# Kernel optimization log

Hardware: AMD Instinct MI355X
Metric: run time of the kernel (lower is better)

Reference implementation:

```python
import jax, jax.numpy as jnp
import numpy as np

B, LQ, LK = 8, 64, 256
E, H, D, NH = 128, 4, 32, 128  # embed_time, num_heads, input_dim, nhidden
EK = E // H


def setup_inputs() -> dict:
    key = jax.random.key(0)
    ks = jax.random.split(key, 10)
    s = 1.0 / np.sqrt(E)
    so = 1.0 / np.sqrt(D * H)
    return {
        "query": jax.random.normal(ks[0], (B, LQ, E), jnp.float32),
        "key": jax.random.normal(ks[1], (B, LK, E), jnp.float32),
        "value": jax.random.normal(ks[2], (B, LK, D), jnp.float32),
        "mask": jax.random.randint(ks[3], (B, LK, D), 0, 2, jnp.int32),
        "Wq": jax.random.uniform(ks[4], (E, E), jnp.float32, -s, s),
        "bq": jax.random.uniform(ks[5], (E,), jnp.float32, -s, s),
        "Wk": jax.random.uniform(ks[6], (E, E), jnp.float32, -s, s),
        "bk": jax.random.uniform(ks[7], (E,), jnp.float32, -s, s),
        "Wo": jax.random.uniform(ks[8], (D * H, NH), jnp.float32, -so, so),
        "bo": jax.random.uniform(ks[9], (NH,), jnp.float32, -so, so),
    }


def reference(query, key, value, mask, Wq, bq, Wk, bk, Wo, bo):
    # project and split heads: [B, L, E] -> [B, H, L, EK]
    q = (query @ Wq + bq).reshape(B, LQ, H, EK).transpose(0, 2, 1, 3)
    k = (key @ Wk + bk).reshape(B, LK, H, EK).transpose(0, 2, 1, 3)
    # scores: [B, H, LQ, LK]
    scores = jnp.einsum("bhqe,bhke->bhqk", q, k) / jnp.sqrt(jnp.asarray(EK, q.dtype))
    # per-feature masked logits: [B, H, LQ, LK, D] (broadcast, matches repeat_interleave)
    m = mask[:, None, None, :, :]  # [B,1,1,LK,D]
    logits = jnp.where(m == 0, jnp.asarray(-1e9, q.dtype), scores[..., None])
    p = jax.nn.softmax(logits, axis=-2)  # softmax over LK, per feature channel
    # weighted sum over LK: [B, H, LQ, D]
    x = jnp.sum(p * value[:, None, None, :, :], axis=-2)
    # merge heads: [B, LQ, H*D]
    x = x.transpose(0, 2, 1, 3).reshape(B, LQ, H * D)
    return x @ Wo + bo
```

## Files before the change

kernel.cpp:

```cpp
#include <hip/hip_runtime.h>

#define B_ 8
#define LQ_ 64
#define LK_ 256
#define E_ 128
#define H_ 4
#define D_ 32
#define NH_ 128
#define EK_ 32

__global__ __launch_bounds__(512, 2) void fused_attn_kernel(
    const float* __restrict__ query, const float* __restrict__ key,
    const float* __restrict__ value, const int* __restrict__ mask,
    const float* __restrict__ Wq, const float* __restrict__ bq,
    const float* __restrict__ Wk,
    const float* __restrict__ Wo, const float* __restrict__ bo,
    float* __restrict__ out)
{
    const int blk = blockIdx.x;
    const int b  = blk >> 5;
    const int q0 = (blk & 31) * 2;
    const int t  = threadIdx.x;

    extern __shared__ float dyn[];
    float* qrow  = dyn;
    float* qpart = dyn + 256;
    float* qp    = dyn + 1280;
    float* g     = dyn + 1536;
    float* kt    = dyn + 2560;
    float* spart = dyn + 2560;
    float* e_lds = dyn + 10752;
    float* nump  = dyn + 12800;
    float* denp  = dyn + 16896;
    float* x     = dyn + 20992;
    float* opart = dyn + 21248;

    {
        const float4* kb4 =
            reinterpret_cast<const float4*>(key + (size_t)b * LK_ * E_);
        #pragma unroll
        for (int i = 0; i < 16; ++i) {
            const int slot = i * 512 + t;
            const int k  = slot >> 5;
            const int p  = slot & 31;
            const float4* src = kb4 + (k * 32 + (p ^ (k & 7)));
            __builtin_amdgcn_global_load_lds(
                (const __attribute__((address_space(1))) void*)src,
                (__attribute__((address_space(3))) void*)(&kt[slot * 4]),
                16, 0, 0);
        }
    }

    const int d  = t & 31;
    const int kg = t >> 5;
    float vv[16], mfv[16];
    {
        const float* vb = value + ((size_t)(b * LK_) + kg * 16) * D_ + d;
        const int*   mb = mask  + ((size_t)(b * LK_) + kg * 16) * D_ + d;
        #pragma unroll
        for (int j = 0; j < 16; ++j) {
            vv[j]  = vb[j * D_];
            mfv[j] = (float)mb[j * D_];
        }
    }

    const int e4 = t >> 2, p4 = t & 3;
    float4 wkr[8];
    {
        const float4* wk4 =
            reinterpret_cast<const float4*>(Wk + (size_t)e4 * E_ + p4 * EK_);
        #pragma unroll
        for (int j = 0; j < 8; ++j) wkr[j] = wk4[j];
    }

    if (t < 64) {
        reinterpret_cast<float4*>(qrow)[t] =
            reinterpret_cast<const float4*>(query + ((size_t)(b * LQ_) + q0) * E_)[t];
    }
    __syncthreads();

    {
        const int col  = t & 127;
        const int slab = t >> 7;
        const float4* qr0 = reinterpret_cast<const float4*>(qrow + slab * 32);
        const float4* qr1 = reinterpret_cast<const float4*>(qrow + 128 + slab * 32);
        const float* wq = Wq + (size_t)(slab * 32) * E_ + col;
        float acc0 = 0.0f, acc1 = 0.0f;
        #pragma unroll
        for (int j = 0; j < 8; ++j) {
            float4 q0v = qr0[j];
            float4 q1v = qr1[j];
            float w0 = wq[(size_t)(j * 4 + 0) * E_];
            float w1 = wq[(size_t)(j * 4 + 1) * E_];
            float w2 = wq[(size_t)(j * 4 + 2) * E_];
            float w3 = wq[(size_t)(j * 4 + 3) * E_];
            acc0 = fmaf(q0v.x, w0, acc0); acc1 = fmaf(q1v.x, w0, acc1);
            acc0 = fmaf(q0v.y, w1, acc0); acc1 = fmaf(q1v.y, w1, acc1);
            acc0 = fmaf(q0v.z, w2, acc0); acc1 = fmaf(q1v.z, w2, acc1);
            acc0 = fmaf(q0v.w, w3, acc0); acc1 = fmaf(q1v.w, w3, acc1);
        }
        qpart[(slab * 2 + 0) * 128 + col] = acc0;
        qpart[(slab * 2 + 1) * 128 + col] = acc1;
    }
    __syncthreads();

    if (t < 256) {
        const int col = t & 127, r = t >> 7;
        float s = bq[col];
        #pragma unroll
        for (int slab = 0; slab < 4; ++slab)
            s += qpart[(slab * 2 + r) * 128 + col];
        qp[r * 128 + col] = s;
    }
    __syncthreads();

    {
        const float inv_sqrt_ek = 0.17677669529663687f;
        #pragma unroll
        for (int r = 0; r < 2; ++r) {
            const float4* qp4 = reinterpret_cast<const float4*>(qp + r * 128 + p4 * EK_);
            float acc = 0.0f;
            #pragma unroll
            for (int j = 0; j < 8; ++j) {
                float4 pv = qp4[j];
                acc = fmaf(wkr[j].x, pv.x, acc);
                acc = fmaf(wkr[j].y, pv.y, acc);
                acc = fmaf(wkr[j].z, pv.z, acc);
                acc = fmaf(wkr[j].w, pv.w, acc);
            }
            g[(r * 4 + p4) * 128 + e4] = acc * inv_sqrt_ek;
        }
    }
    __syncthreads();

    const int k5  = t & 127;
    const int eq5 = t >> 7;
    float acc0[8] = {0.f, 0.f, 0.f, 0.f, 0.f, 0.f, 0.f, 0.f};
    float acc1[8] = {0.f, 0.f, 0.f, 0.f, 0.f, 0.f, 0.f, 0.f};
    {
        const int xr = k5 & 7;
        const float4* kt4 = reinterpret_cast<const float4*>(kt);
        const float4* g4  = reinterpret_cast<const float4*>(g);
        #pragma unroll
        for (int j = 0; j < 8; ++j) {
            const int jj = eq5 * 8 + j;
            const float4 kv0 = kt4[k5 * 32 + (jj ^ xr)];
            const float4 kv1 = kt4[(k5 + 128) * 32 + (jj ^ xr)];
            #pragma unroll
            for (int rh = 0; rh < 8; ++rh) {
                const float4 gg = g4[rh * 32 + jj];
                acc0[rh] = fmaf(kv0.x, gg.x, acc0[rh]);
                acc0[rh] = fmaf(kv0.y, gg.y, acc0[rh]);
                acc0[rh] = fmaf(kv0.z, gg.z, acc0[rh]);
                acc0[rh] = fmaf(kv0.w, gg.w, acc0[rh]);
                acc1[rh] = fmaf(kv1.x, gg.x, acc1[rh]);
                acc1[rh] = fmaf(kv1.y, gg.y, acc1[rh]);
                acc1[rh] = fmaf(kv1.z, gg.z, acc1[rh]);
                acc1[rh] = fmaf(kv1.w, gg.w, acc1[rh]);
            }
        }
    }
    __syncthreads();

    #pragma unroll
    for (int rh = 0; rh < 8; ++rh) {
        spart[(eq5 * 8 + rh) * 256 + k5]       = acc0[rh];
        spart[(eq5 * 8 + rh) * 256 + k5 + 128] = acc1[rh];
    }
    __syncthreads();

    {
        const int w = t >> 6;
        const int l = t & 63;
        const float4* sp4 = reinterpret_cast<const float4*>(spart);
        float4 s0 = sp4[w * 64 + l];
        #pragma unroll
        for (int eq = 1; eq < 4; ++eq) {
            float4 s1 = sp4[(eq * 8 + w) * 64 + l];
            s0.x += s1.x; s0.y += s1.y; s0.z += s1.z; s0.w += s1.w;
        }
        float m = fmaxf(fmaxf(s0.x, s0.y), fmaxf(s0.z, s0.w));
        #pragma unroll
        for (int off = 32; off; off >>= 1)
            m = fmaxf(m, __shfl_xor(m, off));
        float4 e;
        e.x = __expf(s0.x - m); e.y = __expf(s0.y - m);
        e.z = __expf(s0.z - m); e.w = __expf(s0.w - m);
        *reinterpret_cast<float4*>(&e_lds[w * LK_ + l * 4]) = e;
    }
    __syncthreads();

    {
        float num[8] = {0.f, 0.f, 0.f, 0.f, 0.f, 0.f, 0.f, 0.f};
        float den[8] = {0.f, 0.f, 0.f, 0.f, 0.f, 0.f, 0.f, 0.f};
        #pragma unroll
        for (int jq = 0; jq < 4; ++jq) {
            const float4 mv4 = make_float4(mfv[jq*4+0]*vv[jq*4+0], mfv[jq*4+1]*vv[jq*4+1],
                                           mfv[jq*4+2]*vv[jq*4+2], mfv[jq*4+3]*vv[jq*4+3]);
            const float4 mf4 = make_float4(mfv[jq*4+0], mfv[jq*4+1],
                                           mfv[jq*4+2], mfv[jq*4+3]);
            #pragma unroll
            for (int rh = 0; rh < 8; ++rh) {
                float4 ev = *reinterpret_cast<const float4*>(
                    &e_lds[rh * LK_ + kg * 16 + jq * 4]);
                num[rh] = fmaf(ev.x, mv4.x, num[rh]);
                num[rh] = fmaf(ev.y, mv4.y, num[rh]);
                num[rh] = fmaf(ev.z, mv4.z, num[rh]);
                num[rh] = fmaf(ev.w, mv4.w, num[rh]);
                den[rh] = fmaf(ev.x, mf4.x, den[rh]);
                den[rh] = fmaf(ev.y, mf4.y, den[rh]);
                den[rh] = fmaf(ev.z, mf4.z, den[rh]);
                den[rh] = fmaf(ev.w, mf4.w, den[rh]);
            }
        }
        #pragma unroll
        for (int rh = 0; rh < 8; ++rh) {
            nump[(kg * 8 + rh) * 32 + d] = num[rh];
            denp[(kg * 8 + rh) * 32 + d] = den[rh];
        }
    }
    __syncthreads();

    if (t < 256) {
        const int rh = t >> 5, dd = t & 31;
        float n = 0.f, dn = 0.f;
        #pragma unroll
        for (int k2 = 0; k2 < 16; ++k2) {
            n  += nump[(k2 * 8 + rh) * 32 + dd];
            dn += denp[(k2 * 8 + rh) * 32 + dd];
        }
        x[(rh >> 2) * 128 + (rh & 3) * 32 + dd] = n / dn;
    }
    __syncthreads();

    {
        const int col = t & 127;
        const int eq  = t >> 7;
        const int c0  = eq * 32;
        const float* wo = Wo + (size_t)c0 * NH_ + col;
        const float4* x40 = reinterpret_cast<const float4*>(x + c0);
        const float4* x41 = reinterpret_cast<const float4*>(x + 128 + c0);
        float acc0o = 0.f, acc1o = 0.f;
        #pragma unroll
        for (int j = 0; j < 8; ++j) {
            float4 xv0 = x40[j];
            float4 xv1 = x41[j];
            float w0 = wo[(size_t)(j * 4 + 0) * NH_];
            float w1 = wo[(size_t)(j * 4 + 1) * NH_];
            float w2 = wo[(size_t)(j * 4 + 2) * NH_];
            float w3 = wo[(size_t)(j * 4 + 3) * NH_];
            acc0o = fmaf(xv0.x, w0, acc0o); acc1o = fmaf(xv1.x, w0, acc1o);
            acc0o = fmaf(xv0.y, w1, acc0o); acc1o = fmaf(xv1.y, w1, acc1o);
            acc0o = fmaf(xv0.z, w2, acc0o); acc1o = fmaf(xv1.z, w2, acc1o);
            acc0o = fmaf(xv0.w, w3, acc0o); acc1o = fmaf(xv1.w, w3, acc1o);
        }
        opart[(eq * 2 + 0) * 128 + col] = acc0o;
        opart[(eq * 2 + 1) * 128 + col] = acc1o;
    }
    __syncthreads();

    if (t < 256) {
        const int col = t & 127, r = t >> 7;
        float s = bo[col];
        #pragma unroll
        for (int eq = 0; eq < 4; ++eq)
            s += opart[(eq * 2 + r) * 128 + col];
        out[((size_t)(b * LQ_) + q0 + r) * NH_ + col] = s;
    }
}

extern "C" void kernel_launch(void* const* d_in, const int* in_sizes, int n_in,
                              void* d_out, int out_size, void* d_ws, size_t ws_size,
                              hipStream_t stream) {
    const float* query = (const float*)d_in[0];
    const float* key   = (const float*)d_in[1];
    const float* value = (const float*)d_in[2];
    const int*   mask  = (const int*)d_in[3];
    const float* Wq    = (const float*)d_in[4];
    const float* bq    = (const float*)d_in[5];
    const float* Wk    = (const float*)d_in[6];
    const float* Wo    = (const float*)d_in[8];
    const float* bo    = (const float*)d_in[9];
    float* out = (float*)d_out;

    const size_t lds_bytes = 35328 * sizeof(float);
    static bool attr_set = false;
    if (!attr_set) {
        hipFuncSetAttribute(reinterpret_cast<const void*>(fused_attn_kernel),
                            hipFuncAttributeMaxDynamicSharedMemorySize,
                            (int)lds_bytes);
        attr_set = true;
    }

    fused_attn_kernel<<<B_ * (LQ_ / 2), 512, lds_bytes, stream>>>(
        query, key, value, mask, Wq, bq, Wk, Wo, bo, out);
}
```

Before: 16.32 us.

## Split projections into separate kernel and compute scores from projected keys

Adds a proj_kernel that computes the Q and K projections into workspace: K is scaled by 1/sqrt(EK) and Q gets its bias. The attention kernel then loads the projected K and computes scores as direct per-head dot products. This replaces the per-block folding of Wk into the query (the g vectors), which needed 8 head-row accumulators and a 4-way partial-sum reduction. It removes the K projection work that was redundantly repeated across the 32 query blocks per batch. The cost is a second kernel launch and a global round trip through workspace, and the fused kernel remains as a fallback when no workspace is given. It also drops the bk bias, relying on the fact that adding bk shifts each score row by a constant that softmax cancels.

```diff
diff --git a/kernel.cpp b/kernel.cpp
--- a/kernel.cpp
+++ b/kernel.cpp
@@ -9,11 +9,61 @@
 #define NH_ 128
 #define EK_ 32
 
-__global__ __launch_bounds__(512, 2) void fused_attn_kernel(
-    const float* __restrict__ query, const float* __restrict__ key,
+#define SCALE_EK 0.17677669529663687f
+
+
+__global__ __launch_bounds__(256, 4) void proj_kernel(
+    const float* __restrict__ key, const float* __restrict__ query,
+    const float* __restrict__ Wk, const float* __restrict__ Wq,
+    const float* __restrict__ bq,
+    float* __restrict__ kp, float* __restrict__ qp)
+{
+    const int blkrow = blockIdx.x * 4;
+    const int t = threadIdx.x;
+    const bool is_q = blkrow >= (B_ * LK_);
+    const float* in = is_q ? (query + (size_t)(blkrow - B_ * LK_) * E_)
+                           : (key + (size_t)blkrow * E_);
+    const float* W = is_q ? Wq : Wk;
+
+    __shared__ float in_lds[4 * E_];
+    if (t < 128)
+        reinterpret_cast<float4*>(in_lds)[t] =
+            reinterpret_cast<const float4*>(in)[t];
+    __syncthreads();
+
+    const int col = t & 127;
+    const int rr  = t >> 7;
+    const float4* i40 = reinterpret_cast<const float4*>(in_lds + rr * E_);
+    const float4* i41 = reinterpret_cast<const float4*>(in_lds + (rr + 2) * E_);
+    float acc0 = 0.f, acc1 = 0.f;
+    #pragma unroll
+    for (int jf = 0; jf < 32; ++jf) {
+        const float4 a0 = i40[jf];
+        const float4 a1 = i41[jf];
+        const float* wr = W + (size_t)(jf * 4) * E_ + col;
+        const float w0 = wr[0];
+        const float w1 = wr[E_];
+        const float w2 = wr[2 * E_];
+        const float w3 = wr[3 * E_];
+        acc0 = fmaf(a0.x, w0, acc0); acc1 = fmaf(a1.x, w0, acc1);
+        acc0 = fmaf(a0.y, w1, acc0); acc1 = fmaf(a1.y, w1, acc1);
+        acc0 = fmaf(a0.z, w2, acc0); acc1 = fmaf(a1.z, w2, acc1);
+        acc0 = fmaf(a0.w, w3, acc0); acc1 = fmaf(a1.w, w3, acc1);
+    }
+    if (is_q) {
+        const int r0 = blkrow - B_ * LK_;
+        const float bb = bq[col];
+        qp[(size_t)(r0 + rr) * E_ + col]     = acc0 + bb;
+        qp[(size_t)(r0 + rr + 2) * E_ + col] = acc1 + bb;
+    } else {
+        kp[(size_t)(blkrow + rr) * E_ + col]     = acc0 * SCALE_EK;
+        kp[(size_t)(blkrow + rr + 2) * E_ + col] = acc1 * SCALE_EK;
+    }
+}
+
+__global__ __launch_bounds__(512, 2) void attn_kernel(
+    const float* __restrict__ kp, const float* __restrict__ qp_g,
     const float* __restrict__ value, const int* __restrict__ mask,
-    const float* __restrict__ Wq, const float* __restrict__ bq,
-    const float* __restrict__ Wk,
     const float* __restrict__ Wo, const float* __restrict__ bo,
     float* __restrict__ out)
 {
@@ -23,26 +73,23 @@
     const int t  = threadIdx.x;
 
     extern __shared__ float dyn[];
-    float* qrow  = dyn;
-    float* qpart = dyn + 256;
-    float* qp    = dyn + 1280;
-    float* g     = dyn + 1536;
-    float* kt    = dyn + 2560;
-    float* spart = dyn + 2560;
-    float* e_lds = dyn + 10752;
-    float* nump  = dyn + 12800;
-    float* denp  = dyn + 16896;
-    float* x     = dyn + 20992;
-    float* opart = dyn + 21248;
+    float* qp_lds = dyn;
+    float* s_lds  = dyn + 256;
+    float* kt     = dyn + 2560;
+    float* e_lds  = dyn + 2560;
+    float* nump   = dyn + 4608;
+    float* denp   = dyn + 8704;
+    float* x      = dyn + 12800;
+    float* opart  = dyn + 13056;
 
     {
         const float4* kb4 =
-            reinterpret_cast<const float4*>(key + (size_t)b * LK_ * E_);
+            reinterpret_cast<const float4*>(kp + (size_t)b * LK_ * E_);
         #pragma unroll
         for (int i = 0; i < 16; ++i) {
             const int slot = i * 512 + t;
-            const int k  = slot >> 5;
-            const int p  = slot & 31;
+            const int k = slot >> 5;
+            const int p = slot & 31;
             const float4* src = kb4 + (k * 32 + (p ^ (k & 7)));
             __builtin_amdgcn_global_load_lds(
                 (const __attribute__((address_space(1))) void*)src,
@@ -64,121 +111,47 @@
         }
     }
 
-    const int e4 = t >> 2, p4 = t & 3;
-    float4 wkr[8];
-    {
-        const float4* wk4 =
-            reinterpret_cast<const float4*>(Wk + (size_t)e4 * E_ + p4 * EK_);
-        #pragma unroll
-        for (int j = 0; j < 8; ++j) wkr[j] = wk4[j];
-    }
-
     if (t < 64) {
-        reinterpret_cast<float4*>(qrow)[t] =
-            reinterpret_cast<const float4*>(query + ((size_t)(b * LQ_) + q0) * E_)[t];
-    }
-    __syncthreads();
-
-    {
-        const int col  = t & 127;
-        const int slab = t >> 7;
-        const float4* qr0 = reinterpret_cast<const float4*>(qrow + slab * 32);
-        const float4* qr1 = reinterpret_cast<const float4*>(qrow + 128 + slab * 32);
-        const float* wq = Wq + (size_t)(slab * 32) * E_ + col;
-        float acc0 = 0.0f, acc1 = 0.0f;
-        #pragma unroll
-        for (int j = 0; j < 8; ++j) {
-            float4 q0v = qr0[j];
-            float4 q1v = qr1[j];
-            float w0 = wq[(size_t)(j * 4 + 0) * E_];
-            float w1 = wq[(size_t)(j * 4 + 1) * E_];
-            float w2 = wq[(size_t)(j * 4 + 2) * E_];
-            float w3 = wq[(size_t)(j * 4 + 3) * E_];
-            acc0 = fmaf(q0v.x, w0, acc0); acc1 = fmaf(q1v.x, w0, acc1);
-            acc0 = fmaf(q0v.y, w1, acc0); acc1 = fmaf(q1v.y, w1, acc1);
-            acc0 = fmaf(q0v.z, w2, acc0); acc1 = fmaf(q1v.z, w2, acc1);
-            acc0 = fmaf(q0v.w, w3, acc0); acc1 = fmaf(q1v.w, w3, acc1);
-        }
-        qpart[(slab * 2 + 0) * 128 + col] = acc0;
-        qpart[(slab * 2 + 1) * 128 + col] = acc1;
-    }
-    __syncthreads();
-
-    if (t < 256) {
-        const int col = t & 127, r = t >> 7;
-        float s = bq[col];
-        #pragma unroll
-        for (int slab = 0; slab < 4; ++slab)
-            s += qpart[(slab * 2 + r) * 128 + col];
-        qp[r * 128 + col] = s;
-    }
-    __syncthreads();
-
-    {
-        const float inv_sqrt_ek = 0.17677669529663687f;
-        #pragma unroll
-        for (int r = 0; r < 2; ++r) {
-            const float4* qp4 = reinterpret_cast<const float4*>(qp + r * 128 + p4 * EK_);
-            float acc = 0.0f;
-            #pragma unroll
-            for (int j = 0; j < 8; ++j) {
-                float4 pv = qp4[j];
-                acc = fmaf(wkr[j].x, pv.x, acc);
-                acc = fmaf(wkr[j].y, pv.y, acc);
-                acc = fmaf(wkr[j].z, pv.z, acc);
-                acc = fmaf(wkr[j].w, pv.w, acc);
-            }
-            g[(r * 4 + p4) * 128 + e4] = acc * inv_sqrt_ek;
-        }
-    }
-    __syncthreads();
-
-    const int k5  = t & 127;
-    const int eq5 = t >> 7;
-    float acc0[8] = {0.f, 0.f, 0.f, 0.f, 0.f, 0.f, 0.f, 0.f};
-    float acc1[8] = {0.f, 0.f, 0.f, 0.f, 0.f, 0.f, 0.f, 0.f};
-    {
+        reinterpret_cast<float4*>(qp_lds)[t] =
+            reinterpret_cast<const float4*>(qp_g + ((size_t)(b * LQ_) + q0) * E_)[t];
+    }
+    __syncthreads();
+
+    {
+        const int k5 = t & 127;
+        const int h5 = t >> 7;
         const int xr = k5 & 7;
         const float4* kt4 = reinterpret_cast<const float4*>(kt);
-        const float4* g4  = reinterpret_cast<const float4*>(g);
+        const float4* q40 = reinterpret_cast<const float4*>(qp_lds + h5 * EK_);
+        const float4* q41 = reinterpret_cast<const float4*>(qp_lds + 128 + h5 * EK_);
+        float a00 = 0.f, a01 = 0.f, a10 = 0.f, a11 = 0.f;
         #pragma unroll
         for (int j = 0; j < 8; ++j) {
-            const int jj = eq5 * 8 + j;
+            const int jj = h5 * 8 + j;
             const float4 kv0 = kt4[k5 * 32 + (jj ^ xr)];
             const float4 kv1 = kt4[(k5 + 128) * 32 + (jj ^ xr)];
-            #pragma unroll
-            for (int rh = 0; rh < 8; ++rh) {
-                const float4 gg = g4[rh * 32 + jj];
-                acc0[rh] = fmaf(kv0.x, gg.x, acc0[rh]);
-                acc0[rh] = fmaf(kv0.y, gg.y, acc0[rh]);
-                acc0[rh] = fmaf(kv0.z, gg.z, acc0[rh]);
-                acc0[rh] = fmaf(kv0.w, gg.w, acc0[rh]);
-                acc1[rh] = fmaf(kv1.x, gg.x, acc1[rh]);
-                acc1[rh] = fmaf(kv1.y, gg.y, acc1[rh]);
-                acc1[rh] = fmaf(kv1.z, gg.z, acc1[rh]);
-                acc1[rh] = fmaf(kv1.w, gg.w, acc1[rh]);
-            }
-        }
-    }
-    __syncthreads();
-
-    #pragma unroll
-    for (int rh = 0; rh < 8; ++rh) {
-        spart[(eq5 * 8 + rh) * 256 + k5]       = acc0[rh];
-        spart[(eq5 * 8 + rh) * 256 + k5 + 128] = acc1[rh];
+            const float4 qa = q40[j];
+            const float4 qb = q41[j];
+            a00 = fmaf(kv0.x, qa.x, a00); a01 = fmaf(kv1.x, qa.x, a01);
+            a00 = fmaf(kv0.y, qa.y, a00); a01 = fmaf(kv1.y, qa.y, a01);
+            a00 = fmaf(kv0.z, qa.z, a00); a01 = fmaf(kv1.z, qa.z, a01);
+            a00 = fmaf(kv0.w, qa.w, a00); a01 = fmaf(kv1.w, qa.w, a01);
+            a10 = fmaf(kv0.x, qb.x, a10); a11 = fmaf(kv1.x, qb.x, a11);
+            a10 = fmaf(kv0.y, qb.y, a10); a11 = fmaf(kv1.y, qb.y, a11);
+            a10 = fmaf(kv0.z, qb.z, a10); a11 = fmaf(kv1.z, qb.z, a11);
+            a10 = fmaf(kv0.w, qb.w, a10); a11 = fmaf(kv1.w, qb.w, a11);
+        }
+        s_lds[h5 * 256 + k5]             = a00;
+        s_lds[h5 * 256 + k5 + 128]       = a01;
+        s_lds[(4 + h5) * 256 + k5]       = a10;
+        s_lds[(4 + h5) * 256 + k5 + 128] = a11;
     }
     __syncthreads();
 
     {
         const int w = t >> 6;
         const int l = t & 63;
-        const float4* sp4 = reinterpret_cast<const float4*>(spart);
-        float4 s0 = sp4[w * 64 + l];
-        #pragma unroll
-        for (int eq = 1; eq < 4; ++eq) {
-            float4 s1 = sp4[(eq * 8 + w) * 64 + l];
-            s0.x += s1.x; s0.y += s1.y; s0.z += s1.z; s0.w += s1.w;
-        }
+        float4 s0 = *reinterpret_cast<const float4*>(&s_lds[w * 256 + l * 4]);
         float m = fmaxf(fmaxf(s0.x, s0.y), fmaxf(s0.z, s0.w));
         #pragma unroll
         for (int off = 32; off; off >>= 1)
@@ -240,6 +213,266 @@
         const float* wo = Wo + (size_t)c0 * NH_ + col;
         const float4* x40 = reinterpret_cast<const float4*>(x + c0);
         const float4* x41 = reinterpret_cast<const float4*>(x + 128 + c0);
+        float acc0 = 0.f, acc1 = 0.f;
+        #pragma unroll
+        for (int j = 0; j < 8; ++j) {
+            float4 xv0 = x40[j];
+            float4 xv1 = x41[j];
+            float w0 = wo[(size_t)(j * 4 + 0) * NH_];
+            float w1 = wo[(size_t)(j * 4 + 1) * NH_];
+            float w2 = wo[(size_t)(j * 4 + 2) * NH_];
+            float w3 = wo[(size_t)(j * 4 + 3) * NH_];
+            acc0 = fmaf(xv0.x, w0, acc0); acc1 = fmaf(xv1.x, w0, acc1);
+            acc0 = fmaf(xv0.y, w1, acc0); acc1 = fmaf(xv1.y, w1, acc1);
+            acc0 = fmaf(xv0.z, w2, acc0); acc1 = fmaf(xv1.z, w2, acc1);
+            acc0 = fmaf(xv0.w, w3, acc0); acc1 = fmaf(xv1.w, w3, acc1);
+        }
+        opart[(eq * 2 + 0) * 128 + col] = acc0;
+        opart[(eq * 2 + 1) * 128 + col] = acc1;
+    }
+    __syncthreads();
+
+    if (t < 256) {
+        const int col = t & 127, r = t >> 7;
+        float s = bo[col];
+        #pragma unroll
+        for (int eq = 0; eq < 4; ++eq)
+            s += opart[(eq * 2 + r) * 128 + col];
+        out[((size_t)(b * LQ_) + q0 + r) * NH_ + col] = s;
+    }
+}
+
+__global__ __launch_bounds__(512, 2) void fused_attn_kernel(
+    const float* __restrict__ query, const float* __restrict__ key,
+    const float* __restrict__ value, const int* __restrict__ mask,
+    const float* __restrict__ Wq, const float* __restrict__ bq,
+    const float* __restrict__ Wk,
+    const float* __restrict__ Wo, const float* __restrict__ bo,
+    float* __restrict__ out)
+{
+    const int blk = blockIdx.x;
+    const int b  = blk >> 5;
+    const int q0 = (blk & 31) * 2;
+    const int t  = threadIdx.x;
+
+    extern __shared__ float dyn[];
+    float* qrow  = dyn;
+    float* qpart = dyn + 256;
+    float* qp    = dyn + 1280;
+    float* g     = dyn + 1536;
+    float* kt    = dyn + 2560;
+    float* spart = dyn + 2560;
+    float* e_lds = dyn + 10752;
+    float* nump  = dyn + 12800;
+    float* denp  = dyn + 16896;
+    float* x     = dyn + 20992;
+    float* opart = dyn + 21248;
+
+    {
+        const float4* kb4 =
+            reinterpret_cast<const float4*>(key + (size_t)b * LK_ * E_);
+        #pragma unroll
+        for (int i = 0; i < 16; ++i) {
+            const int slot = i * 512 + t;
+            const int k  = slot >> 5;
+            const int p  = slot & 31;
+            const float4* src = kb4 + (k * 32 + (p ^ (k & 7)));
+            __builtin_amdgcn_global_load_lds(
+                (const __attribute__((address_space(1))) void*)src,
+                (__attribute__((address_space(3))) void*)(&kt[slot * 4]),
+                16, 0, 0);
+        }
+    }
+
+    const int d  = t & 31;
+    const int kg = t >> 5;
+    float vv[16], mfv[16];
+    {
+        const float* vb = value + ((size_t)(b * LK_) + kg * 16) * D_ + d;
+        const int*   mb = mask  + ((size_t)(b * LK_) + kg * 16) * D_ + d;
+        #pragma unroll
+        for (int j = 0; j < 16; ++j) {
+            vv[j]  = vb[j * D_];
+            mfv[j] = (float)mb[j * D_];
+        }
+    }
+
+    const int e4 = t >> 2, p4 = t & 3;
+    float4 wkr[8];
+    {
+        const float4* wk4 =
+            reinterpret_cast<const float4*>(Wk + (size_t)e4 * E_ + p4 * EK_);
+        #pragma unroll
+        for (int j = 0; j < 8; ++j) wkr[j] = wk4[j];
+    }
+
+    if (t < 64) {
+        reinterpret_cast<float4*>(qrow)[t] =
+            reinterpret_cast<const float4*>(query + ((size_t)(b * LQ_) + q0) * E_)[t];
+    }
+    __syncthreads();
+
+    {
+        const int col  = t & 127;
+        const int slab = t >> 7;
+        const float4* qr0 = reinterpret_cast<const float4*>(qrow + slab * 32);
+        const float4* qr1 = reinterpret_cast<const float4*>(qrow + 128 + slab * 32);
+        const float* wq = Wq + (size_t)(slab * 32) * E_ + col;
+        float acc0 = 0.0f, acc1 = 0.0f;
+        #pragma unroll
+        for (int j = 0; j < 8; ++j) {
+            float4 q0v = qr0[j];
+            float4 q1v = qr1[j];
+            float w0 = wq[(size_t)(j * 4 + 0) * E_];
+            float w1 = wq[(size_t)(j * 4 + 1) * E_];
+            float w2 = wq[(size_t)(j * 4 + 2) * E_];
+            float w3 = wq[(size_t)(j * 4 + 3) * E_];
+            acc0 = fmaf(q0v.x, w0, acc0); acc1 = fmaf(q1v.x, w0, acc1);
+            acc0 = fmaf(q0v.y, w1, acc0); acc1 = fmaf(q1v.y, w1, acc1);
+            acc0 = fmaf(q0v.z, w2, acc0); acc1 = fmaf(q1v.z, w2, acc1);
+            acc0 = fmaf(q0v.w, w3, acc0); acc1 = fmaf(q1v.w, w3, acc1);
+        }
+        qpart[(slab * 2 + 0) * 128 + col] = acc0;
+        qpart[(slab * 2 + 1) * 128 + col] = acc1;
+    }
+    __syncthreads();
+
+    if (t < 256) {
+        const int col = t & 127, r = t >> 7;
+        float s = bq[col];
+        #pragma unroll
+        for (int slab = 0; slab < 4; ++slab)
+            s += qpart[(slab * 2 + r) * 128 + col];
+        qp[r * 128 + col] = s;
+    }
+    __syncthreads();
+
+    {
+        const float inv_sqrt_ek = 0.17677669529663687f;
+        #pragma unroll
+        for (int r = 0; r < 2; ++r) {
+            const float4* qp4 = reinterpret_cast<const float4*>(qp + r * 128 + p4 * EK_);
+            float acc = 0.0f;
+            #pragma unroll
+            for (int j = 0; j < 8; ++j) {
+                float4 pv = qp4[j];
+                acc = fmaf(wkr[j].x, pv.x, acc);
+                acc = fmaf(wkr[j].y, pv.y, acc);
+                acc = fmaf(wkr[j].z, pv.z, acc);
+                acc = fmaf(wkr[j].w, pv.w, acc);
+            }
+            g[(r * 4 + p4) * 128 + e4] = acc * inv_sqrt_ek;
+        }
+    }
+    __syncthreads();
+
+    const int k5  = t & 127;
+    const int eq5 = t >> 7;
+    float acc0[8] = {0.f, 0.f, 0.f, 0.f, 0.f, 0.f, 0.f, 0.f};
+    float acc1[8] = {0.f, 0.f, 0.f, 0.f, 0.f, 0.f, 0.f, 0.f};
+    {
+        const int xr = k5 & 7;
+        const float4* kt4 = reinterpret_cast<const float4*>(kt);
+        const float4* g4  = reinterpret_cast<const float4*>(g);
+        #pragma unroll
+        for (int j = 0; j < 8; ++j) {
+            const int jj = eq5 * 8 + j;
+            const float4 kv0 = kt4[k5 * 32 + (jj ^ xr)];
+            const float4 kv1 = kt4[(k5 + 128) * 32 + (jj ^ xr)];
+            #pragma unroll
+            for (int rh = 0; rh < 8; ++rh) {
+                const float4 gg = g4[rh * 32 + jj];
+                acc0[rh] = fmaf(kv0.x, gg.x, acc0[rh]);
+                acc0[rh] = fmaf(kv0.y, gg.y, acc0[rh]);
+                acc0[rh] = fmaf(kv0.z, gg.z, acc0[rh]);
+                acc0[rh] = fmaf(kv0.w, gg.w, acc0[rh]);
+                acc1[rh] = fmaf(kv1.x, gg.x, acc1[rh]);
+                acc1[rh] = fmaf(kv1.y, gg.y, acc1[rh]);
+                acc1[rh] = fmaf(kv1.z, gg.z, acc1[rh]);
+                acc1[rh] = fmaf(kv1.w, gg.w, acc1[rh]);
+            }
+        }
+    }
+    __syncthreads();
+
+    #pragma unroll
+    for (int rh = 0; rh < 8; ++rh) {
+        spart[(eq5 * 8 + rh) * 256 + k5]       = acc0[rh];
+        spart[(eq5 * 8 + rh) * 256 + k5 + 128] = acc1[rh];
+    }
+    __syncthreads();
+
+    {
+        const int w = t >> 6;
+        const int l = t & 63;
+        const float4* sp4 = reinterpret_cast<const float4*>(spart);
+        float4 s0 = sp4[w * 64 + l];
+        #pragma unroll
+        for (int eq = 1; eq < 4; ++eq) {
+            float4 s1 = sp4[(eq * 8 + w) * 64 + l];
+            s0.x += s1.x; s0.y += s1.y; s0.z += s1.z; s0.w += s1.w;
+        }
+        float m = fmaxf(fmaxf(s0.x, s0.y), fmaxf(s0.z, s0.w));
+        #pragma unroll
+        for (int off = 32; off; off >>= 1)
+            m = fmaxf(m, __shfl_xor(m, off));
+        float4 e;
+        e.x = __expf(s0.x - m); e.y = __expf(s0.y - m);
+        e.z = __expf(s0.z - m); e.w = __expf(s0.w - m);
+        *reinterpret_cast<float4*>(&e_lds[w * LK_ + l * 4]) = e;
+    }
+    __syncthreads();
+
+    {
+        float num[8] = {0.f, 0.f, 0.f, 0.f, 0.f, 0.f, 0.f, 0.f};
+        float den[8] = {0.f, 0.f, 0.f, 0.f, 0.f, 0.f, 0.f, 0.f};
+        #pragma unroll
+        for (int jq = 0; jq < 4; ++jq) {
+            const float4 mv4 = make_float4(mfv[jq*4+0]*vv[jq*4+0], mfv[jq*4+1]*vv[jq*4+1],
+                                           mfv[jq*4+2]*vv[jq*4+2], mfv[jq*4+3]*vv[jq*4+3]);
+            const float4 mf4 = make_float4(mfv[jq*4+0], mfv[jq*4+1],
+                                           mfv[jq*4+2], mfv[jq*4+3]);
+            #pragma unroll
+            for (int rh = 0; rh < 8; ++rh) {
+                float4 ev = *reinterpret_cast<const float4*>(
+                    &e_lds[rh * LK_ + kg * 16 + jq * 4]);
+                num[rh] = fmaf(ev.x, mv4.x, num[rh]);
+                num[rh] = fmaf(ev.y, mv4.y, num[rh]);
+                num[rh] = fmaf(ev.z, mv4.z, num[rh]);
+                num[rh] = fmaf(ev.w, mv4.w, num[rh]);
+                den[rh] = fmaf(ev.x, mf4.x, den[rh]);
+                den[rh] = fmaf(ev.y, mf4.y, den[rh]);
+                den[rh] = fmaf(ev.z, mf4.z, den[rh]);
+                den[rh] = fmaf(ev.w, mf4.w, den[rh]);
+            }
+        }
+        #pragma unroll
+        for (int rh = 0; rh < 8; ++rh) {
+            nump[(kg * 8 + rh) * 32 + d] = num[rh];
+            denp[(kg * 8 + rh) * 32 + d] = den[rh];
+        }
+    }
+    __syncthreads();
+
+    if (t < 256) {
+        const int rh = t >> 5, dd = t & 31;
+        float n = 0.f, dn = 0.f;
+        #pragma unroll
+        for (int k2 = 0; k2 < 16; ++k2) {
+            n  += nump[(k2 * 8 + rh) * 32 + dd];
+            dn += denp[(k2 * 8 + rh) * 32 + dd];
+        }
+        x[(rh >> 2) * 128 + (rh & 3) * 32 + dd] = n / dn;
+    }
+    __syncthreads();
+
+    {
+        const int col = t & 127;
+        const int eq  = t >> 7;
+        const int c0  = eq * 32;
+        const float* wo = Wo + (size_t)c0 * NH_ + col;
+        const float4* x40 = reinterpret_cast<const float4*>(x + c0);
+        const float4* x41 = reinterpret_cast<const float4*>(x + 128 + c0);
         float acc0o = 0.f, acc1o = 0.f;
         #pragma unroll
         for (int j = 0; j < 8; ++j) {
@@ -284,14 +517,28 @@
     float* out = (float*)d_out;
 
     const size_t lds_bytes = 35328 * sizeof(float);
+    const size_t ws_needed = (size_t)(B_ * LK_ + B_ * LQ_) * E_ * sizeof(float);
+
     static bool attr_set = false;
     if (!attr_set) {
+        hipFuncSetAttribute(reinterpret_cast<const void*>(attn_kernel),
+                            hipFuncAttributeMaxDynamicSharedMemorySize,
+                            (int)lds_bytes);
         hipFuncSetAttribute(reinterpret_cast<const void*>(fused_attn_kernel),
                             hipFuncAttributeMaxDynamicSharedMemorySize,
                             (int)lds_bytes);
         attr_set = true;
     }
 
-    fused_attn_kernel<<<B_ * (LQ_ / 2), 512, lds_bytes, stream>>>(
-        query, key, value, mask, Wq, bq, Wk, Wo, bo, out);
+    if (d_ws != nullptr && ws_size >= ws_needed) {
+        float* kp = (float*)d_ws;
+        float* qp = kp + (size_t)B_ * LK_ * E_;
+        proj_kernel<<<(B_ * (LK_ + LQ_)) / 4, 256, 0, stream>>>(
+            key, query, Wk, Wq, bq, kp, qp);
+        attn_kernel<<<B_ * (LQ_ / 2), 512, lds_bytes, stream>>>(
+            kp, qp, value, mask, Wo, bo, out);
+    } else {
+        fused_attn_kernel<<<B_ * (LQ_ / 2), 512, lds_bytes, stream>>>(
+            query, key, value, mask, Wq, bq, Wk, Wo, bo, out);
+    }
 }
```

After: 18.01 us. 10.4% more time.

## Prefetch Wq/Wo weights into registers early, remap blocks, use raw barriers

Applied to the files above, without the earlier changes.

The Wq and Wo column slices are loaded into registers at kernel start, and the query row is loaded alongside the key-to-LDS copy, so the global latency of these loads overlaps instead of sitting on the critical path of each projection. The block index is permuted so that consecutive blocks spread across batches. Several __syncthreads are replaced with an inline s_waitcnt lgkmcnt(0)+s_barrier that does not wait on outstanding vector memory loads, which lets the in-flight global_load_lds key copy continue through the early barriers. The cost is 64 extra live registers per thread under launch_bounds(512,2), which risks spills, and the raw barrier relies on the LDS-loaded key data being waited on correctly later.

```diff
diff --git a/kernel.cpp b/kernel.cpp
--- a/kernel.cpp
+++ b/kernel.cpp
@@ -9,6 +9,9 @@
 #define NH_ 128
 #define EK_ 32
 
+
+#define RAW_BARRIER() asm volatile("s_waitcnt lgkmcnt(0)\n\ts_barrier" ::: "memory")
+
 __global__ __launch_bounds__(512, 2) void fused_attn_kernel(
     const float* __restrict__ query, const float* __restrict__ key,
     const float* __restrict__ value, const int* __restrict__ mask,
@@ -17,7 +20,8 @@
     const float* __restrict__ Wo, const float* __restrict__ bo,
     float* __restrict__ out)
 {
-    const int blk = blockIdx.x;
+    const int blk0 = blockIdx.x;
+    const int blk  = (blk0 & 7) * 32 + (blk0 >> 3);
     const int b  = blk >> 5;
     const int q0 = (blk & 31) * 2;
     const int t  = threadIdx.x;
@@ -35,14 +39,37 @@
     float* x     = dyn + 20992;
     float* opart = dyn + 21248;
 
+    float4 qv0;
+    if (t < 64)
+        qv0 = reinterpret_cast<const float4*>(
+            query + ((size_t)(b * LQ_) + q0) * E_)[t];
+
+    const int col2  = t & 127;
+    const int slab2 = t >> 7;
+    float wqr[32];
+    {
+        const float* wqp = Wq + (size_t)(slab2 * 32) * E_ + col2;
+        #pragma unroll
+        for (int j = 0; j < 32; ++j) wqr[j] = wqp[(size_t)j * E_];
+    }
+
+    const int e4 = t >> 2, p4 = t & 3;
+    float4 wkr[8];
+    {
+        const float4* wk4 =
+            reinterpret_cast<const float4*>(Wk + (size_t)e4 * E_ + p4 * EK_);
+        #pragma unroll
+        for (int j = 0; j < 8; ++j) wkr[j] = wk4[j];
+    }
+
     {
         const float4* kb4 =
             reinterpret_cast<const float4*>(key + (size_t)b * LK_ * E_);
         #pragma unroll
         for (int i = 0; i < 16; ++i) {
             const int slot = i * 512 + t;
-            const int k  = slot >> 5;
-            const int p  = slot & 31;
+            const int k = slot >> 5;
+            const int p = slot & 31;
             const float4* src = kb4 + (k * 32 + (p ^ (k & 7)));
             __builtin_amdgcn_global_load_lds(
                 (const __attribute__((address_space(1))) void*)src,
@@ -64,45 +91,39 @@
         }
     }
 
-    const int e4 = t >> 2, p4 = t & 3;
-    float4 wkr[8];
-    {
-        const float4* wk4 =
-            reinterpret_cast<const float4*>(Wk + (size_t)e4 * E_ + p4 * EK_);
-        #pragma unroll
-        for (int j = 0; j < 8; ++j) wkr[j] = wk4[j];
+    float wor[32];
+    {
+        const float* wop = Wo + (size_t)(slab2 * 32) * NH_ + col2;
+        #pragma unroll
+        for (int j = 0; j < 32; ++j) wor[j] = wop[(size_t)j * NH_];
     }
 
     if (t < 64) {
-        reinterpret_cast<float4*>(qrow)[t] =
-            reinterpret_cast<const float4*>(query + ((size_t)(b * LQ_) + q0) * E_)[t];
-    }
-    __syncthreads();
-
-    {
-        const int col  = t & 127;
-        const int slab = t >> 7;
-        const float4* qr0 = reinterpret_cast<const float4*>(qrow + slab * 32);
-        const float4* qr1 = reinterpret_cast<const float4*>(qrow + 128 + slab * 32);
-        const float* wq = Wq + (size_t)(slab * 32) * E_ + col;
+        reinterpret_cast<float4*>(qrow)[t] = qv0;
+    }
+    RAW_BARRIER();
+
+    {
+        const float4* qr0 = reinterpret_cast<const float4*>(qrow + slab2 * 32);
+        const float4* qr1 = reinterpret_cast<const float4*>(qrow + 128 + slab2 * 32);
         float acc0 = 0.0f, acc1 = 0.0f;
         #pragma unroll
         for (int j = 0; j < 8; ++j) {
             float4 q0v = qr0[j];
             float4 q1v = qr1[j];
-            float w0 = wq[(size_t)(j * 4 + 0) * E_];
-            float w1 = wq[(size_t)(j * 4 + 1) * E_];
-            float w2 = wq[(size_t)(j * 4 + 2) * E_];
-            float w3 = wq[(size_t)(j * 4 + 3) * E_];
+            const float w0 = wqr[j * 4 + 0];
+            const float w1 = wqr[j * 4 + 1];
+            const float w2 = wqr[j * 4 + 2];
+            const float w3 = wqr[j * 4 + 3];
             acc0 = fmaf(q0v.x, w0, acc0); acc1 = fmaf(q1v.x, w0, acc1);
             acc0 = fmaf(q0v.y, w1, acc0); acc1 = fmaf(q1v.y, w1, acc1);
             acc0 = fmaf(q0v.z, w2, acc0); acc1 = fmaf(q1v.z, w2, acc1);
             acc0 = fmaf(q0v.w, w3, acc0); acc1 = fmaf(q1v.w, w3, acc1);
         }
-        qpart[(slab * 2 + 0) * 128 + col] = acc0;
-        qpart[(slab * 2 + 1) * 128 + col] = acc1;
-    }
-    __syncthreads();
+        qpart[(slab2 * 2 + 0) * 128 + col2] = acc0;
+        qpart[(slab2 * 2 + 1) * 128 + col2] = acc1;
+    }
+    RAW_BARRIER();
 
     if (t < 256) {
         const int col = t & 127, r = t >> 7;
@@ -112,7 +133,7 @@
             s += qpart[(slab * 2 + r) * 128 + col];
         qp[r * 128 + col] = s;
     }
-    __syncthreads();
+    RAW_BARRIER();
 
     {
         const float inv_sqrt_ek = 0.17677669529663687f;
@@ -234,10 +255,7 @@
     __syncthreads();
 
     {
-        const int col = t & 127;
-        const int eq  = t >> 7;
-        const int c0  = eq * 32;
-        const float* wo = Wo + (size_t)c0 * NH_ + col;
+        const int c0 = slab2 * 32;
         const float4* x40 = reinterpret_cast<const float4*>(x + c0);
         const float4* x41 = reinterpret_cast<const float4*>(x + 128 + c0);
         float acc0o = 0.f, acc1o = 0.f;
@@ -245,17 +263,17 @@
         for (int j = 0; j < 8; ++j) {
             float4 xv0 = x40[j];
             float4 xv1 = x41[j];
-            float w0 = wo[(size_t)(j * 4 + 0) * NH_];
-            float w1 = wo[(size_t)(j * 4 + 1) * NH_];
-            float w2 = wo[(size_t)(j * 4 + 2) * NH_];
-            float w3 = wo[(size_t)(j * 4 + 3) * NH_];
+            const float w0 = wor[j * 4 + 0];
+            const float w1 = wor[j * 4 + 1];
+            const float w2 = wor[j * 4 + 2];
+            const float w3 = wor[j * 4 + 3];
             acc0o = fmaf(xv0.x, w0, acc0o); acc1o = fmaf(xv1.x, w0, acc1o);
             acc0o = fmaf(xv0.y, w1, acc0o); acc1o = fmaf(xv1.y, w1, acc1o);
             acc0o = fmaf(xv0.z, w2, acc0o); acc1o = fmaf(xv1.z, w2, acc1o);
             acc0o = fmaf(xv0.w, w3, acc0o); acc1o = fmaf(xv1.w, w3, acc1o);
         }
-        opart[(eq * 2 + 0) * 128 + col] = acc0o;
-        opart[(eq * 2 + 1) * 128 + col] = acc1o;
+        opart[(slab2 * 2 + 0) * 128 + col2] = acc0o;
+        opart[(slab2 * 2 + 1) * 128 + col2] = acc1o;
     }
     __syncthreads();
 
```

Result: no change. 16.16 us, median of 2 (-0.9%).
